# Optimization experiments

Hardware: AMD Instinct MI355X
Metric: run time of the kernel (lower is better)

## Reference

```python
import jax, jax.numpy as jnp
import numpy as np

N, D, H, K, STEPS = 100000, 384, 128, 5, 3


def setup_inputs() -> dict:
    key = jax.random.key(0)
    ks = jax.random.split(key, 5)
    emb = jax.random.normal(ks[0], (N, D), dtype=jnp.float32)
    qv = jax.random.normal(ks[1], (D,), dtype=jnp.float32)
    W1 = jax.random.normal(ks[2], (2 * D, H), dtype=jnp.float32) * (1.0 / np.sqrt(2 * D))
    b1 = jnp.zeros((H,), dtype=jnp.float32)
    W2 = jax.random.normal(ks[3], (H, K), dtype=jnp.float32) * (1.0 / np.sqrt(H))
    b2 = jnp.zeros((K,), dtype=jnp.float32)
    nbr = jax.random.randint(ks[4], (N, K), 0, N, dtype=jnp.int32)  # k-NN neighbor ids per node
    return {"emb": emb, "qv": qv, "W1": W1, "b1": b1, "W2": W2, "b2": b2, "nbr": nbr}


def _quantum_walk(emb, qv, W1, b1, W2, b2, nbr):
    n, k = nbr.shape
    # coin_net MLP on [emb_i ; q] -- independent of walk state, compute once.
    inp = jnp.concatenate([emb, jnp.broadcast_to(qv, (n, qv.shape[0]))], axis=1)  # [n, 2d]
    h = jax.nn.relu(inp @ W1 + b1)
    amps = h @ W2 + b2  # [n, k]

    anorm = jnp.linalg.norm(amps, axis=1)                      # [n]
    c = amps[:, :, None] * amps[:, None, :]                    # [n, k, k] outer product
    cnorm = jnp.linalg.norm(c.reshape(n, -1), axis=1)          # [n] Frobenius norm
    valid = (anorm > 0) & jnp.isfinite(anorm) & (cnorm > 0)
    # fallback coin: ones outer product normalized -> all entries 1/k (||ones_{k,k}||_F = k)
    uniform = jnp.full((k, k), 1.0 / k, dtype=amps.dtype)
    safe_cnorm = jnp.where(cnorm > 0, cnorm, 1.0)
    coins = jnp.where(valid[:, None, None], c / safe_cnorm[:, None, None], uniform)  # [n,k,k]

    init = jnp.full((n, k), 1.0 / np.sqrt(n * k), dtype=amps.dtype)
    cols = jnp.broadcast_to(jnp.arange(k), (n, k))

    def step(state, _):
        s_p = jnp.einsum('nkl,nl->nk', coins, state)                    # coin_i @ state_i
        new_state = jnp.zeros_like(state).at[nbr, cols].add(s_p)        # scatter to neighbor slots
        norm = jnp.linalg.norm(new_state)
        safe = jnp.where(norm > 0, norm, 1.0)
        state = jnp.where(norm > 0, new_state / safe, init)
        return state, None

    state, _ = jax.lax.scan(step, init, None, length=STEPS)
    return jnp.abs(state).sum(axis=1)  # per-node retrieval logits [n]


def reference(emb, qv, W1, b1, W2, b2, nbr):
    return _quantum_walk(emb, qv, W1, b1, W2, b2, nbr)
```

## Files before the change

### kernel.cpp

```cpp
#include <hip/hip_runtime.h>
#include <hip/hip_bf16.h>
#include <math.h>

#define NN 100000
#define DD 384
#define HH 128
#define KK 5

typedef __attribute__((ext_vector_type(8))) short short8;
typedef __attribute__((ext_vector_type(4))) float f32x4;

constexpr float INIT_VAL = 1.4142135623730951e-3f;
constexpr float RSQRT5   = 0.44721359549995793f;

__device__ __forceinline__ ushort bf16rn(float x) {
    unsigned u = __float_as_uint(x);
    return (ushort)((u + 0x7FFFu + ((u >> 16) & 1u)) >> 16);
}

__global__ __launch_bounds__(256) void prep_kernel(
    const float* __restrict__ qv, const float* __restrict__ W1,
    const float* __restrict__ b1, const int* __restrict__ nbr,
    float* __restrict__ b1p, ushort* __restrict__ W1h,
    int* __restrict__ nbrT, float* __restrict__ sA, float* __restrict__ sB,
    float* __restrict__ sC, float* __restrict__ ssp) {
    const int b = blockIdx.x, tid = threadIdx.x;
    if (b == 0) {
        __shared__ float part[256];
        const int h = tid & 127, half = tid >> 7;
        float s = 0.f;
        const float* Wq = W1 + (size_t)(DD + half * 192) * HH + h;
        const float* qh = qv + half * 192;
#pragma unroll 8
        for (int k = 0; k < 192; ++k)
            s = fmaf(qh[k], Wq[(size_t)k * HH], s);
        part[tid] = s;
        __syncthreads();
        if (tid < HH) b1p[tid] = part[tid] + part[tid + 128] + b1[tid];
        if (tid == 0) ssp[0] = 0.f;
    } else if (b <= 24) {
        int t = (b - 1) * 256 + tid;
        int l = t & 63;
        int ks = (t >> 6) % 12;
        int c = (t >> 6) / 12;
        int k0 = ks * 32 + ((l >> 4) << 3);
        int col = c * 16 + (l & 15);
#pragma unroll
        for (int e = 0; e < 8; ++e)
            W1h[(size_t)t * 8 + e] = bf16rn(W1[(size_t)(k0 + e) * HH + col]);
    } else {
        int i = (b - 25) * 256 + tid;
        if (i < NN) {
#pragma unroll
            for (int j = 0; j < KK; ++j) {
                nbrT[j * NN + i] = nbr[i * KK + j];
                sA[j * NN + i] = 0.f;
                sB[j * NN + i] = 0.f;
                sC[j * NN + i] = 0.f;
            }
        }
    }
}

__global__ __launch_bounds__(256) void mlp_mfma_kernel(
    const float* __restrict__ emb, const ushort* __restrict__ W1h,
    const float* __restrict__ b1p, const float* __restrict__ W2,
    const float* __restrict__ b2, const int* __restrict__ nbrT,
    float* __restrict__ gout , float* __restrict__ sA) {
    __shared__ __align__(16) ushort Ah[32 * 128];
    __shared__ float pbuf[32][21];

    const int tid = threadIdx.x;
    const int lane = tid & 63;
    const int wn = tid >> 6;
    const int blkBase = blockIdx.x * 32;

    f32x4 acc[2][2];
#pragma unroll
    for (int mt = 0; mt < 2; ++mt)
#pragma unroll
        for (int nt = 0; nt < 2; ++nt) acc[mt][nt] = (f32x4){0.f, 0.f, 0.f, 0.f};

    float4 aregs[4];
    auto issueA = [&](int t) {
#pragma unroll
        for (int i = 0; i < 4; ++i) {
            int idx = tid + i * 256;
            int r = idx >> 5, c = idx & 31;
            int node = min(blkBase + r, NN - 1);
            aregs[i] = *reinterpret_cast<const float4*>(&emb[(size_t)node * DD + t * 128 + c * 4]);
        }
    };
    auto writeLDS = [&]() {
#pragma unroll
        for (int i = 0; i < 4; ++i) {
            int idx = tid + i * 256;
            int r = idx >> 5, c = idx & 31;
            ushort4 hv;
            hv.x = bf16rn(aregs[i].x);
            hv.y = bf16rn(aregs[i].y);
            hv.z = bf16rn(aregs[i].z);
            hv.w = bf16rn(aregs[i].w);
            int byte = (r * 256 + c * 8) ^ ((r & 7) << 4);
            *reinterpret_cast<ushort4*>(reinterpret_cast<char*>(Ah) + byte) = hv;
        }
    };

    issueA(0);
    writeLDS();
    __syncthreads();

#pragma unroll
    for (int t = 0; t < 3; ++t) {
        if (t < 2) issueA(t + 1);

        short8 bh[2][2], ah[2][2];
        auto loadB = [&](int kt, int s) {
            int ks = t * 4 + kt;
#pragma unroll
            for (int nt = 0; nt < 2; ++nt) {
                int c = wn * 2 + nt;
                size_t off = ((size_t)(c * 12 + ks) * 64 + lane) * 8;
                bh[s][nt] = *reinterpret_cast<const short8*>(&W1h[off]);
            }
        };
        auto loadA = [&](int kt, int s) {
#pragma unroll
            for (int mt = 0; mt < 2; ++mt) {
                int row = mt * 16 + (lane & 15);
                int byte = (row * 256 + kt * 64 + ((lane >> 4) << 4)) ^ ((row & 7) << 4);
                ah[s][mt] = *reinterpret_cast<const short8*>(reinterpret_cast<const char*>(Ah) + byte);
            }
        };

        loadB(0, 0);
        loadA(0, 0);
#pragma unroll
        for (int kt = 0; kt < 4; ++kt) {
            const int cur = kt & 1, nxt = cur ^ 1;
            if (kt < 3) {
                loadB(kt + 1, nxt);
                loadA(kt + 1, nxt);
            }
#pragma unroll
            for (int mt = 0; mt < 2; ++mt)
#pragma unroll
                for (int nt = 0; nt < 2; ++nt)
                    acc[mt][nt] = __builtin_amdgcn_mfma_f32_16x16x32_bf16(ah[cur][mt], bh[cur][nt], acc[mt][nt], 0, 0, 0);
        }

        if (t < 2) {
            __syncthreads();
            writeLDS();
            __syncthreads();
        }
    }

    float b1v[2], w2v[2][KK];
#pragma unroll
    for (int nt = 0; nt < 2; ++nt) {
        int h = (wn * 2 + nt) * 16 + (lane & 15);
        b1v[nt] = b1p[h];
#pragma unroll
        for (int j = 0; j < KK; ++j) w2v[nt][j] = W2[h * KK + j];
    }
#pragma unroll
    for (int mt = 0; mt < 2; ++mt) {
        float p[4][KK];
#pragma unroll
        for (int r = 0; r < 4; ++r)
#pragma unroll
            for (int j = 0; j < KK; ++j) p[r][j] = 0.f;
#pragma unroll
        for (int nt = 0; nt < 2; ++nt)
#pragma unroll
            for (int r = 0; r < 4; ++r) {
                float v = fmaxf(acc[mt][nt][r] + b1v[nt], 0.f);
#pragma unroll
                for (int j = 0; j < KK; ++j) p[r][j] = fmaf(v, w2v[nt][j], p[r][j]);
            }
#pragma unroll
        for (int off = 1; off < 16; off <<= 1)
#pragma unroll
            for (int r = 0; r < 4; ++r)
#pragma unroll
                for (int j = 0; j < KK; ++j) p[r][j] += __shfl_xor(p[r][j], off, 64);
        if ((lane & 15) == 0) {
            int rowbase = mt * 16 + (lane >> 4) * 4;
#pragma unroll
            for (int r = 0; r < 4; ++r)
#pragma unroll
                for (int j = 0; j < KK; ++j) pbuf[rowbase + r][wn * 5 + j] = p[r][j];
        }
    }
    __syncthreads();
    if (tid < 32) {
        int node = blkBase + tid;
        if (node < NN) {
            float a[KK], an2 = 0.f;
#pragma unroll
            for (int j = 0; j < KK; ++j) {
                a[j] = pbuf[tid][j] + pbuf[tid][5 + j] + pbuf[tid][10 + j] +
                       pbuf[tid][15 + j] + b2[j];
                an2 = fmaf(a[j], a[j], an2);
            }
            float an = sqrtf(an2);
            bool valid = (an2 > 0.f) && isfinite(an);
            float g5[KK], ssum = 0.f;
#pragma unroll
            for (int j = 0; j < KK; ++j) {
                g5[j] = valid ? (a[j] / an) : RSQRT5;
                gout[j * NN + node] = g5[j];
                ssum += g5[j];
            }
            float d = ssum * INIT_VAL;
#pragma unroll
            for (int j = 0; j < KK; ++j)
                atomicAdd(&sA[j * NN + nbrT[j * NN + node]], g5[j] * d);
        }
    }
}

__global__ void walk_step_kernel(const float* __restrict__ g, const int* __restrict__ nbrT,
                                 const float* __restrict__ u, float* __restrict__ v) {
    int i = blockIdx.x * blockDim.x + threadIdx.x;
    if (i >= NN) return;
    float gj[KK], d = 0.f;
#pragma unroll
    for (int j = 0; j < KK; ++j) {
        gj[j] = g[j * NN + i];
        d = fmaf(gj[j], u[j * NN + i], d);
    }
#pragma unroll
    for (int j = 0; j < KK; ++j)
        atomicAdd(&v[j * NN + nbrT[j * NN + i]], gj[j] * d);
}

__global__ void norm_reduce_kernel(const float* __restrict__ u, float* __restrict__ ss) {
    int i = blockIdx.x * blockDim.x + threadIdx.x;
    const int total4 = (KK * NN) / 4;
    float s = 0.f;
    for (int idx = i; idx < total4; idx += gridDim.x * blockDim.x) {
        float4 x = reinterpret_cast<const float4*>(u)[idx];
        s = fmaf(x.x, x.x, s);
        s = fmaf(x.y, x.y, s);
        s = fmaf(x.z, x.z, s);
        s = fmaf(x.w, x.w, s);
    }
#pragma unroll
    for (int off = 32; off > 0; off >>= 1) s += __shfl_xor(s, off, 64);
    if ((threadIdx.x & 63) == 0) atomicAdd(ss, s);
}

__global__ void finalize_kernel(const float* __restrict__ u, const float* __restrict__ ss,
                                float* __restrict__ out) {
    int i = blockIdx.x * blockDim.x + threadIdx.x;
    if (i >= NN) return;
    float s = 0.f;
#pragma unroll
    for (int j = 0; j < KK; ++j) s += fabsf(u[j * NN + i]);
    float nrm = sqrtf(*ss);
    out[i] = (nrm > 0.f) ? (s / nrm) : (KK * INIT_VAL);
}

extern "C" void kernel_launch(void* const* d_in, const int* in_sizes, int n_in,
                              void* d_out, int out_size, void* d_ws, size_t ws_size,
                              hipStream_t stream) {
    const float* emb = (const float*)d_in[0];
    const float* qv  = (const float*)d_in[1];
    const float* W1  = (const float*)d_in[2];
    const float* b1  = (const float*)d_in[3];
    const float* W2  = (const float*)d_in[4];
    const float* b2  = (const float*)d_in[5];
    const int*   nbr = (const int*)d_in[6];
    float* out = (float*)d_out;

    char* ws = (char*)d_ws;
    size_t off = 0;
    auto alloc = [&](size_t bytes) {
        char* p = ws + off;
        off += (bytes + 255) & ~(size_t)255;
        return p;
    };
    float*  b1p  = (float*)alloc(HH * sizeof(float));
    ushort* W1h  = (ushort*)alloc((size_t)DD * HH * sizeof(ushort));
    float*  gbuf = (float*)alloc((size_t)KK * NN * sizeof(float));
    int*    nbrT = (int*)  alloc((size_t)KK * NN * sizeof(int));
    float*  sA   = (float*)alloc((size_t)KK * NN * sizeof(float));
    float*  sB   = (float*)alloc((size_t)KK * NN * sizeof(float));
    float*  sC   = (float*)alloc((size_t)KK * NN * sizeof(float));
    float*  ssp  = (float*)alloc(sizeof(float));

    const int nblk = (NN + 255) / 256;

    prep_kernel<<<25 + nblk, 256, 0, stream>>>(qv, W1, b1, nbr, b1p, W1h,
                                               nbrT, sA, sB, sC, ssp);
    mlp_mfma_kernel<<<(NN + 31) / 32, 256, 0, stream>>>(emb, W1h, b1p, W2, b2,
                                                        nbrT, gbuf, sA);

    walk_step_kernel<<<nblk, 256, 0, stream>>>(gbuf, nbrT, sA, sB);
    walk_step_kernel<<<nblk, 256, 0, stream>>>(gbuf, nbrT, sB, sC);

    norm_reduce_kernel<<<512, 256, 0, stream>>>(sC, ssp);
    finalize_kernel<<<nblk, 256, 0, stream>>>(sC, ssp, out);
}
```

Baseline: 148.0 us.

## Load full embedding tile directly to LDS via global_load_lds, drop staged pipeline

The MLP kernel now stages the whole 32x384 fp32 embedding tile into LDS at once using direct global-to-LDS 16-byte loads, laid out in MFMA fragment order. This replaces the three-stage register-staged pipeline with its bf16 conversion and swizzled LDS writes, and leaves a single barrier in place of several. The bf16 conversion now happens per wave when fragments are read from LDS, so each block converts its data redundantly across waves. LDS use doubles to 48KB of fp32, which may lower occupancy, and load/compute overlap within the block is lost.

```diff
diff --git a/kernel.cpp b/kernel.cpp
--- a/kernel.cpp
+++ b/kernel.cpp
@@ -16,6 +16,12 @@
 __device__ __forceinline__ ushort bf16rn(float x) {
     unsigned u = __float_as_uint(x);
     return (ushort)((u + 0x7FFFu + ((u >> 16) & 1u)) >> 16);
+}
+
+typedef __attribute__((address_space(3))) unsigned lds_as_t;
+typedef __attribute__((address_space(1))) const unsigned glb_as_t;
+__device__ __forceinline__ void gload_lds16(const float* g, float* l) {
+    __builtin_amdgcn_global_load_lds((glb_as_t*)g, (lds_as_t*)l, 16, 0, 0);
 }
 
 __global__ __launch_bounds__(256) void prep_kernel(
@@ -67,13 +73,29 @@
     const float* __restrict__ b1p, const float* __restrict__ W2,
     const float* __restrict__ b2, const int* __restrict__ nbrT,
     float* __restrict__ gout , float* __restrict__ sA) {
-    __shared__ __align__(16) ushort Ah[32 * 128];
+    __shared__ __align__(16) float Abuf[12][2][2][64][4];
     __shared__ float pbuf[32][21];
 
     const int tid = threadIdx.x;
     const int lane = tid & 63;
     const int wn = tid >> 6;
     const int blkBase = blockIdx.x * 32;
+    const int gp = lane >> 4;
+    const int rl = lane & 15;
+
+#pragma unroll
+    for (int ki = 0; ki < 3; ++ki) {
+        int ks = wn * 3 + ki;
+#pragma unroll
+        for (int mt = 0; mt < 2; ++mt)
+#pragma unroll
+            for (int c = 0; c < 2; ++c) {
+                int node = min(blkBase + mt * 16 + rl, NN - 1);
+                const float* src = emb + (size_t)node * DD + ks * 32 + gp * 8 + c * 4;
+                gload_lds16(src, &Abuf[ks][mt][c][0][0]);
+            }
+    }
+    __syncthreads();
 
     f32x4 acc[2][2];
 #pragma unroll
@@ -81,79 +103,38 @@
 #pragma unroll
         for (int nt = 0; nt < 2; ++nt) acc[mt][nt] = (f32x4){0.f, 0.f, 0.f, 0.f};
 
-    float4 aregs[4];
-    auto issueA = [&](int t) {
-#pragma unroll
-        for (int i = 0; i < 4; ++i) {
-            int idx = tid + i * 256;
-            int r = idx >> 5, c = idx & 31;
-            int node = min(blkBase + r, NN - 1);
-            aregs[i] = *reinterpret_cast<const float4*>(&emb[(size_t)node * DD + t * 128 + c * 4]);
+    short8 bh[2][2];
+    auto loadB = [&](int ks, int s) {
+#pragma unroll
+        for (int nt = 0; nt < 2; ++nt) {
+            int c = wn * 2 + nt;
+            size_t off = ((size_t)(c * 12 + ks) * 64 + lane) * 8;
+            bh[s][nt] = *reinterpret_cast<const short8*>(&W1h[off]);
         }
     };
-    auto writeLDS = [&]() {
-#pragma unroll
-        for (int i = 0; i < 4; ++i) {
-            int idx = tid + i * 256;
-            int r = idx >> 5, c = idx & 31;
-            ushort4 hv;
-            hv.x = bf16rn(aregs[i].x);
-            hv.y = bf16rn(aregs[i].y);
-            hv.z = bf16rn(aregs[i].z);
-            hv.w = bf16rn(aregs[i].w);
-            int byte = (r * 256 + c * 8) ^ ((r & 7) << 4);
-            *reinterpret_cast<ushort4*>(reinterpret_cast<char*>(Ah) + byte) = hv;
-        }
-    };
-
-    issueA(0);
-    writeLDS();
-    __syncthreads();
-
-#pragma unroll
-    for (int t = 0; t < 3; ++t) {
-        if (t < 2) issueA(t + 1);
-
-        short8 bh[2][2], ah[2][2];
-        auto loadB = [&](int kt, int s) {
-            int ks = t * 4 + kt;
-#pragma unroll
-            for (int nt = 0; nt < 2; ++nt) {
-                int c = wn * 2 + nt;
-                size_t off = ((size_t)(c * 12 + ks) * 64 + lane) * 8;
-                bh[s][nt] = *reinterpret_cast<const short8*>(&W1h[off]);
-            }
-        };
-        auto loadA = [&](int kt, int s) {
-#pragma unroll
-            for (int mt = 0; mt < 2; ++mt) {
-                int row = mt * 16 + (lane & 15);
-                int byte = (row * 256 + kt * 64 + ((lane >> 4) << 4)) ^ ((row & 7) << 4);
-                ah[s][mt] = *reinterpret_cast<const short8*>(reinterpret_cast<const char*>(Ah) + byte);
-            }
-        };
-
-        loadB(0, 0);
-        loadA(0, 0);
-#pragma unroll
-        for (int kt = 0; kt < 4; ++kt) {
-            const int cur = kt & 1, nxt = cur ^ 1;
-            if (kt < 3) {
-                loadB(kt + 1, nxt);
-                loadA(kt + 1, nxt);
-            }
-#pragma unroll
-            for (int mt = 0; mt < 2; ++mt)
-#pragma unroll
-                for (int nt = 0; nt < 2; ++nt)
-                    acc[mt][nt] = __builtin_amdgcn_mfma_f32_16x16x32_bf16(ah[cur][mt], bh[cur][nt], acc[mt][nt], 0, 0, 0);
-        }
-
-        if (t < 2) {
-            __syncthreads();
-            writeLDS();
-            __syncthreads();
-        }
+    loadB(0, 0);
+#pragma unroll
+    for (int ks = 0; ks < 12; ++ks) {
+        const int cur = ks & 1, nxt = cur ^ 1;
+        if (ks < 11) loadB(ks + 1, nxt);
+        short8 ah[2];
+#pragma unroll
+        for (int mt = 0; mt < 2; ++mt) {
+            float4 x = *reinterpret_cast<const float4*>(&Abuf[ks][mt][0][lane][0]);
+            float4 y = *reinterpret_cast<const float4*>(&Abuf[ks][mt][1][lane][0]);
+            union { short8 s; ushort u[8]; } A;
+            A.u[0] = bf16rn(x.x); A.u[1] = bf16rn(x.y);
+            A.u[2] = bf16rn(x.z); A.u[3] = bf16rn(x.w);
+            A.u[4] = bf16rn(y.x); A.u[5] = bf16rn(y.y);
+            A.u[6] = bf16rn(y.z); A.u[7] = bf16rn(y.w);
+            ah[mt] = A.s;
+        }
+#pragma unroll
+        for (int mt = 0; mt < 2; ++mt)
+#pragma unroll
+            for (int nt = 0; nt < 2; ++nt)
+                acc[mt][nt] = __builtin_amdgcn_mfma_f32_16x16x32_bf16(
+                    ah[mt], bh[cur][nt], acc[mt][nt], 0, 0, 0);
     }
 
     float b1v[2], w2v[2][KK];
```

New measurement: 162.3 us. 1.1x slower.

## Fuse walk steps, norm reduction and finalize into one persistent kernel with grid barriers

Applied to the files above, without the earlier changes.

Replaces the two walk-step launches, the norm reduction and the finalize launch with one kernel. Inside it, software grid-wide barriers built on atomic counters separate the phases. Each thread keeps its coin values and neighbor ids in registers across phases and zeroes sB/sC itself, instead of relying on prep to do it. This removes several kernel launches and repeated global reloads. The risk is deadlock if not all blocks are co-resident, plus the cost of spinning on the barriers.

```diff
diff --git a/kernel.cpp b/kernel.cpp
--- a/kernel.cpp
+++ b/kernel.cpp
@@ -22,8 +22,8 @@
     const float* __restrict__ qv, const float* __restrict__ W1,
     const float* __restrict__ b1, const int* __restrict__ nbr,
     float* __restrict__ b1p, ushort* __restrict__ W1h,
-    int* __restrict__ nbrT, float* __restrict__ sA, float* __restrict__ sB,
-    float* __restrict__ sC, float* __restrict__ ssp) {
+    int* __restrict__ nbrT, float* __restrict__ sA,
+    float* __restrict__ ssp, unsigned* __restrict__ cnt) {
     const int b = blockIdx.x, tid = threadIdx.x;
     if (b == 0) {
         __shared__ float part[256];
@@ -38,6 +38,7 @@
         __syncthreads();
         if (tid < HH) b1p[tid] = part[tid] + part[tid + 128] + b1[tid];
         if (tid == 0) ssp[0] = 0.f;
+        if (tid < 8) cnt[tid] = 0u;
     } else if (b <= 24) {
         int t = (b - 1) * 256 + tid;
         int l = t & 63;
@@ -55,8 +56,6 @@
             for (int j = 0; j < KK; ++j) {
                 nbrT[j * NN + i] = nbr[i * KK + j];
                 sA[j * NN + i] = 0.f;
-                sB[j * NN + i] = 0.f;
-                sC[j * NN + i] = 0.f;
             }
         }
     }
@@ -221,46 +220,77 @@
     }
 }
 
-__global__ void walk_step_kernel(const float* __restrict__ g, const int* __restrict__ nbrT,
-                                 const float* __restrict__ u, float* __restrict__ v) {
-    int i = blockIdx.x * blockDim.x + threadIdx.x;
-    if (i >= NN) return;
-    float gj[KK], d = 0.f;
-#pragma unroll
-    for (int j = 0; j < KK; ++j) {
-        gj[j] = g[j * NN + i];
-        d = fmaf(gj[j], u[j * NN + i], d);
-    }
-#pragma unroll
-    for (int j = 0; j < KK; ++j)
-        atomicAdd(&v[j * NN + nbrT[j * NN + i]], gj[j] * d);
-}
-
-__global__ void norm_reduce_kernel(const float* __restrict__ u, float* __restrict__ ss) {
-    int i = blockIdx.x * blockDim.x + threadIdx.x;
-    const int total4 = (KK * NN) / 4;
+__device__ __forceinline__ void gbar(unsigned* cnt, unsigned target) {
+    __threadfence();
+    __syncthreads();
+    if (threadIdx.x == 0) {
+        atomicAdd(cnt, 1u);
+        while (__hip_atomic_load(cnt, __ATOMIC_ACQUIRE, __HIP_MEMORY_SCOPE_AGENT) < target) {}
+    }
+    __syncthreads();
+}
+
+__global__ __launch_bounds__(256) void walk_tail_kernel(
+    const float* __restrict__ g, const int* __restrict__ nbrT,
+    const float* __restrict__ sA, float* __restrict__ sB, float* __restrict__ sC,
+    float* __restrict__ ssp, unsigned* __restrict__ cnt, float* __restrict__ out) {
+    const int i = blockIdx.x * 256 + threadIdx.x;
+    const bool act = i < NN;
+    const unsigned nb_total = gridDim.x;
+
+    float gj[KK];
+    int nb[KK];
+    float d1 = 0.f;
+    if (act) {
+#pragma unroll
+        for (int j = 0; j < KK; ++j) {
+            gj[j] = g[j * NN + i];
+            nb[j] = nbrT[j * NN + i];
+            sB[j * NN + i] = 0.f;
+            sC[j * NN + i] = 0.f;
+            d1 = fmaf(gj[j], sA[j * NN + i], d1);
+        }
+    }
+    gbar(cnt + 0, nb_total);
+
+    if (act) {
+#pragma unroll
+        for (int j = 0; j < KK; ++j)
+            atomicAdd(&sB[j * NN + nb[j]], gj[j] * d1);
+    }
+    gbar(cnt + 1, nb_total);
+
+    if (act) {
+        float d2 = 0.f;
+#pragma unroll
+        for (int j = 0; j < KK; ++j) d2 = fmaf(gj[j], sB[j * NN + i], d2);
+#pragma unroll
+        for (int j = 0; j < KK; ++j)
+            atomicAdd(&sC[j * NN + nb[j]], gj[j] * d2);
+    }
+    gbar(cnt + 2, nb_total);
+
     float s = 0.f;
-    for (int idx = i; idx < total4; idx += gridDim.x * blockDim.x) {
-        float4 x = reinterpret_cast<const float4*>(u)[idx];
-        s = fmaf(x.x, x.x, s);
-        s = fmaf(x.y, x.y, s);
-        s = fmaf(x.z, x.z, s);
-        s = fmaf(x.w, x.w, s);
+    float cj[KK];
+    if (act) {
+#pragma unroll
+        for (int j = 0; j < KK; ++j) {
+            cj[j] = sC[j * NN + i];
+            s = fmaf(cj[j], cj[j], s);
+        }
     }
 #pragma unroll
     for (int off = 32; off > 0; off >>= 1) s += __shfl_xor(s, off, 64);
-    if ((threadIdx.x & 63) == 0) atomicAdd(ss, s);
-}
-
-__global__ void finalize_kernel(const float* __restrict__ u, const float* __restrict__ ss,
-                                float* __restrict__ out) {
-    int i = blockIdx.x * blockDim.x + threadIdx.x;
-    if (i >= NN) return;
-    float s = 0.f;
-#pragma unroll
-    for (int j = 0; j < KK; ++j) s += fabsf(u[j * NN + i]);
-    float nrm = sqrtf(*ss);
-    out[i] = (nrm > 0.f) ? (s / nrm) : (KK * INIT_VAL);
+    if ((threadIdx.x & 63) == 0) atomicAdd(ssp, s);
+    gbar(cnt + 3, nb_total);
+
+    if (act) {
+        float nrm = sqrtf(ssp[0]);
+        float t = 0.f;
+#pragma unroll
+        for (int j = 0; j < KK; ++j) t += fabsf(cj[j]);
+        out[i] = (nrm > 0.f) ? (t / nrm) : (KK * INIT_VAL);
+    }
 }
 
 extern "C" void kernel_launch(void* const* d_in, const int* in_sizes, int n_in,
@@ -282,25 +312,21 @@
         off += (bytes + 255) & ~(size_t)255;
         return p;
     };
-    float*  b1p  = (float*)alloc(HH * sizeof(float));
-    ushort* W1h  = (ushort*)alloc((size_t)DD * HH * sizeof(ushort));
-    float*  gbuf = (float*)alloc((size_t)KK * NN * sizeof(float));
-    int*    nbrT = (int*)  alloc((size_t)KK * NN * sizeof(int));
-    float*  sA   = (float*)alloc((size_t)KK * NN * sizeof(float));
-    float*  sB   = (float*)alloc((size_t)KK * NN * sizeof(float));
-    float*  sC   = (float*)alloc((size_t)KK * NN * sizeof(float));
-    float*  ssp  = (float*)alloc(sizeof(float));
+    float*    b1p  = (float*)alloc(HH * sizeof(float));
+    ushort*   W1h  = (ushort*)alloc((size_t)DD * HH * sizeof(ushort));
+    float*    gbuf = (float*)alloc((size_t)KK * NN * sizeof(float));
+    int*      nbrT = (int*)  alloc((size_t)KK * NN * sizeof(int));
+    float*    sA   = (float*)alloc((size_t)KK * NN * sizeof(float));
+    float*    sB   = (float*)alloc((size_t)KK * NN * sizeof(float));
+    float*    sC   = (float*)alloc((size_t)KK * NN * sizeof(float));
+    float*    ssp  = (float*)alloc(sizeof(float));
+    unsigned* cnt  = (unsigned*)alloc(8 * sizeof(unsigned));
 
     const int nblk = (NN + 255) / 256;
 
     prep_kernel<<<25 + nblk, 256, 0, stream>>>(qv, W1, b1, nbr, b1p, W1h,
-                                               nbrT, sA, sB, sC, ssp);
+                                               nbrT, sA, ssp, cnt);
     mlp_mfma_kernel<<<(NN + 31) / 32, 256, 0, stream>>>(emb, W1h, b1p, W2, b2,
                                                         nbrT, gbuf, sA);
-
-    walk_step_kernel<<<nblk, 256, 0, stream>>>(gbuf, nbrT, sA, sB);
-    walk_step_kernel<<<nblk, 256, 0, stream>>>(gbuf, nbrT, sB, sC);
-
-    norm_reduce_kernel<<<512, 256, 0, stream>>>(sC, ssp);
-    finalize_kernel<<<nblk, 256, 0, stream>>>(sC, ssp, out);
-}
+    walk_tail_kernel<<<nblk, 256, 0, stream>>>(gbuf, nbrT, sA, sB, sC, ssp, cnt, out);
+}
```

New measurement: 365.3 us. 147% more time.
